# Performance work log

Measured on AMD Instinct MI355X. Metric: run time of the kernel, lower is better.

Reference implementation:

```python
import jax, jax.numpy as jnp
import numpy as np

N, E, F, H, G, C = 50000, 800000, 768, 256, 512, 2  # H = nhid*2 (nhid=128), G graphs, C classes
NHID = 128


def setup_inputs() -> dict:
    key = jax.random.key(0)
    ks = jax.random.split(key, 18)
    s = 0.05
    x = jax.random.normal(ks[0], (N, F), jnp.float32)
    edge_index = jax.random.randint(ks[1], (2, E), 0, N, dtype=jnp.int32)
    # sorted batch vector; every graph non-empty so the 'first node per graph' gather is valid
    batch = ((jnp.arange(N) * G) // N).astype(jnp.int32)
    return {
        "x": x,
        "edge_index": edge_index,
        "batch": batch,
        # GATConv 1 (in=F, out=H, heads=1)
        "W1": jax.random.normal(ks[2], (F, H), jnp.float32) * s,
        "as1": jax.random.normal(ks[3], (H,), jnp.float32) * s,
        "ad1": jax.random.normal(ks[4], (H,), jnp.float32) * s,
        "b1": jnp.zeros((H,), jnp.float32),
        # GATConv 2 (in=H, out=H)
        "W2": jax.random.normal(ks[5], (H, H), jnp.float32) * s,
        "as2": jax.random.normal(ks[6], (H,), jnp.float32) * s,
        "ad2": jax.random.normal(ks[7], (H,), jnp.float32) * s,
        "b2": jnp.zeros((H,), jnp.float32),
        # fc0: num_features -> nhid (news branch)
        "W0": jax.random.normal(ks[8], (F, NHID), jnp.float32) * s,
        "b0": jnp.zeros((NHID,), jnp.float32),
        # fc1: 2*nhid -> nhid (used twice, as in the source)
        "Wf1": jax.random.normal(ks[9], (H, NHID), jnp.float32) * s,
        "bf1": jnp.zeros((NHID,), jnp.float32),
        # fc2: nhid -> num_classes
        "Wf2": jax.random.normal(ks[10], (NHID, C), jnp.float32) * s,
        "bf2": jnp.zeros((C,), jnp.float32),
    }


def _gat(x, src, dst, W, a_s, a_d, b):
    # PyG GATConv, heads=1, concat=True, negative_slope=0.2, self-loops pre-appended to src/dst.
    h = x @ W                                   # [N, H]
    e = jax.nn.leaky_relu((h @ a_s)[src] + (h @ a_d)[dst], 0.2)  # [E+N]
    m = jax.ops.segment_max(e, dst, num_segments=N)
    ex = jnp.exp(e - m[dst])                    # stable segment softmax numerator
    denom = jax.ops.segment_sum(ex, dst, num_segments=N)
    agg = jax.ops.segment_sum(ex[:, None] * h[src], dst, num_segments=N)  # [N, H]
    return agg / denom[:, None] + b


def reference(x, edge_index, batch, W1, as1, ad1, b1, W2, as2, ad2, b2, W0, b0, Wf1, bf1, Wf2, bf2):
    loop = jnp.arange(N, dtype=edge_index.dtype)
    src = jnp.concatenate([edge_index[0], loop])  # add self-loops (PyG default)
    dst = jnp.concatenate([edge_index[1], loop])
    h = jax.nn.selu(_gat(x, src, dst, W1, as1, ad1, b1))
    h = jax.nn.selu(_gat(h, src, dst, W2, as2, ad2, b2))
    # global mean pool over graphs
    cnt = jax.ops.segment_sum(jnp.ones((N,), h.dtype), batch, num_segments=G)
    pooled = jax.nn.selu(jax.ops.segment_sum(h, batch, num_segments=G) / cnt[:, None])
    z = jax.nn.selu(pooled @ Wf1 + bf1)
    # dropout(p=0.5) in eval mode -> identity
    # concat branch: first node of each graph (news root)
    first_idx = jax.ops.segment_min(jnp.arange(N), batch, num_segments=G)
    news = jax.nn.relu(x[first_idx] @ W0 + b0)
    z = jnp.concatenate([z, news], axis=1)       # [G, 2*nhid]
    z = jax.nn.relu(z @ Wf1 + bf1)
    return jax.nn.log_softmax(z @ Wf2 + bf2, axis=-1)
```

## Files before the change

kernel.cpp:

```cpp
#include <hip/hip_runtime.h>
#include <hip/hip_bf16.h>
#include <cstdint>
#include <cstddef>

#define NN 50000
#define EE 800000
#define FF 768
#define HH 256
#define GG 512
#define CC 2
#define NHIDD 128
#define ETOT (EE + NN)
#define NCHUNK 49

typedef __attribute__((ext_vector_type(8))) short bf16x8;
typedef __attribute__((ext_vector_type(4))) float f32x4;
typedef __attribute__((ext_vector_type(8))) unsigned short us8;

__device__ __forceinline__ float b2f(unsigned short u){
  union { float f; uint32_t i; } v; v.i = ((uint32_t)u) << 16; return v.f;
}
__device__ __forceinline__ unsigned short f2b(float f){
  uint32_t u = __float_as_uint(f);
  uint32_t r = (u + 0x7fffu + ((u >> 16) & 1u)) >> 16;
  return (unsigned short)r;
}
__device__ __forceinline__ float selu_f(float x){
  const float lam = 1.0507009873554805f, alp = 1.6732632423543772f;
  return x > 0.f ? lam * x : lam * alp * (__expf(x) - 1.f);
}

__device__ __forceinline__ void gload_lds16(const unsigned short* g, unsigned short* l){
  __builtin_amdgcn_global_load_lds((const __attribute__((address_space(1))) void*)g,
                                   (__attribute__((address_space(3))) void*)l, 16, 0, 0);
}

__global__ __launch_bounds__(256) void xbf_kernel(const float* __restrict__ x, unsigned short* __restrict__ xb){
  size_t i = ((size_t)blockIdx.x * 256 + threadIdx.x) * 8;
  float4 f0 = *(const float4*)&x[i];
  float4 f1 = *(const float4*)&x[i + 4];
  us8 v;
  v[0] = f2b(f0.x); v[1] = f2b(f0.y); v[2] = f2b(f0.z); v[3] = f2b(f0.w);
  v[4] = f2b(f1.x); v[5] = f2b(f1.y); v[6] = f2b(f1.z); v[7] = f2b(f1.w);
  *(us8*)&xb[i] = v;
}

__global__ __launch_bounds__(256) void swizzleW(const float* __restrict__ W,
                                                unsigned short* __restrict__ Wsw, int K){
  int i = blockIdx.x * 256 + threadIdx.x;
  if (i < K * HH){
    int k = i / HH, n = i % HH;
    Wsw[(size_t)(k >> 5) * 8192 + n * 32 + (k & 31)] = f2b(W[i]);
  }
}

__global__ __launch_bounds__(256) void zero_deg(int* deg){
  int i = blockIdx.x * 256 + threadIdx.x;
  if (i < NN) deg[i] = 0;
}

__global__ __launch_bounds__(256) void deg_kernel(const int* __restrict__ dstA, int* __restrict__ deg){
  int i = blockIdx.x * 256 + threadIdx.x;
  if (i < ETOT){
    int d = (i < EE) ? dstA[i] : (i - EE);
    atomicAdd(&deg[d], 1);
  }
}

__global__ __launch_bounds__(256) void scanA(const int* __restrict__ deg, int* __restrict__ bsum){
  __shared__ int red[256];
  int c = blockIdx.x, tid = threadIdx.x;
  int base = c * 1024 + tid * 4;
  int s = 0;
#pragma unroll
  for (int j = 0; j < 4; j++){ int idx = base + j; if (idx < NN) s += deg[idx]; }
  red[tid] = s; __syncthreads();
  for (int off = 128; off > 0; off >>= 1){
    if (tid < off) red[tid] += red[tid + off];
    __syncthreads();
  }
  if (tid == 0) bsum[c] = red[0];
}

__global__ void scanB(int* bsum){
  if (threadIdx.x == 0){
    int run = 0;
    for (int i = 0; i < NCHUNK; i++){ int v = bsum[i]; bsum[i] = run; run += v; }
  }
}

__global__ __launch_bounds__(256) void scanC(const int* __restrict__ deg, const int* __restrict__ bsum,
                                             int* __restrict__ row_ptr, int* __restrict__ fill_ptr){
  __shared__ int ts[256];
  int c = blockIdx.x, tid = threadIdx.x;
  int base = c * 1024 + tid * 4;
  int v[4]; int s = 0;
#pragma unroll
  for (int j = 0; j < 4; j++){ int idx = base + j; v[j] = (idx < NN) ? deg[idx] : 0; s += v[j]; }
  ts[tid] = s; __syncthreads();
  for (int off = 1; off < 256; off <<= 1){
    int add = (tid >= off) ? ts[tid - off] : 0;
    __syncthreads();
    ts[tid] += add;
    __syncthreads();
  }
  int run = ts[tid] - s + bsum[c];
#pragma unroll
  for (int j = 0; j < 4; j++){
    int idx = base + j;
    if (idx < NN){ row_ptr[idx] = run; fill_ptr[idx] = run; }
    run += v[j];
  }
  if (c == 0 && tid == 0) row_ptr[NN] = ETOT;
}

__global__ __launch_bounds__(256) void fill_kernel(const int* __restrict__ srcA, const int* __restrict__ dstA,
                                                   int* __restrict__ fill_ptr, int* __restrict__ csr_src){
  int i = blockIdx.x * 256 + threadIdx.x;
  if (i < ETOT){
    int s = (i < EE) ? srcA[i] : (i - EE);
    int d = (i < EE) ? dstA[i] : (i - EE);
    int pos = atomicAdd(&fill_ptr[d], 1);
    csr_src[pos] = s;
  }
}

template<int K, int MINW>
__global__ __launch_bounds__(256, MINW) void gemm_mfma(const unsigned short* __restrict__ A,
                                                 const unsigned short* __restrict__ Wsw,
                                                 const float* __restrict__ a_s, const float* __restrict__ a_d,
                                                 unsigned short* __restrict__ out,
                                                 float* __restrict__ als, float* __restrict__ ald, int M){
  constexpr int CHROW = K / 8;
  __shared__ unsigned short Al[32 * K];
  const int tid = threadIdx.x;
  const int m0 = blockIdx.x * 32;
  const int lane = tid & 63, w = tid >> 6;
  const int koff = (lane >> 4) * 8;
  const int arow = lane & 15;
  const int nrow = w * 64 + (lane & 15);

  f32x4 acc[2][4];
#pragma unroll
  for (int rt = 0; rt < 2; rt++)
#pragma unroll
    for (int ct = 0; ct < 4; ct++) acc[rt][ct] = (f32x4){0.f, 0.f, 0.f, 0.f};

  constexpr int ROUNDS = (32 * CHROW) / 256;
#pragma unroll
  for (int j = 0; j < ROUNDS; j++){
    int L16 = j * 256 + tid;
    int row = L16 / CHROW;
    int ch  = L16 - row * CHROW;
    int sch = ch ^ (row & 7);
    int gr  = m0 + row; if (gr >= M) gr = M - 1;
    gload_lds16(A + (size_t)gr * K + sch * 8,
                &Al[(size_t)(j * 256 + w * 64) * 8]);
  }

  const unsigned short* bbase = Wsw + ((size_t)nrow * 32 + koff);
  bf16x8 bcur[2][4];
#pragma unroll
  for (int k2 = 0; k2 < 2; k2++)
#pragma unroll
    for (int ct = 0; ct < 4; ct++)
      bcur[k2][ct] = *(const bf16x8*)(bbase + (size_t)k2 * 8192 + ct * 512);

  __syncthreads();

  constexpr int NIT = K / 64;
  for (int ks = 0; ks < NIT; ks++){
    bf16x8 bnext[2][4];
    if (ks + 1 < NIT){
#pragma unroll
      for (int k2 = 0; k2 < 2; k2++)
#pragma unroll
        for (int ct = 0; ct < 4; ct++)
          bnext[k2][ct] = *(const bf16x8*)(bbase + (size_t)((ks + 1) * 2 + k2) * 8192 + ct * 512);
    }
    bf16x8 af[2][2];
#pragma unroll
    for (int k2 = 0; k2 < 2; k2++)
#pragma unroll
      for (int rt = 0; rt < 2; rt++){
        int R = rt * 16 + arow;
        int chb = (ks * 8 + k2 * 4 + (lane >> 4)) ^ (R & 7);
        af[k2][rt] = *(const bf16x8*)&Al[(size_t)R * K + chb * 8];
      }
#pragma unroll
    for (int k2 = 0; k2 < 2; k2++)
#pragma unroll
      for (int rt = 0; rt < 2; rt++)
#pragma unroll
        for (int ct = 0; ct < 4; ct++)
          acc[rt][ct] = __builtin_amdgcn_mfma_f32_16x16x32_bf16(af[k2][rt], bcur[k2][ct], acc[rt][ct], 0, 0, 0);
    if (ks + 1 < NIT){
#pragma unroll
      for (int k2 = 0; k2 < 2; k2++)
#pragma unroll
        for (int ct = 0; ct < 4; ct++) bcur[k2][ct] = bnext[k2][ct];
    }
  }

#pragma unroll
  for (int rt = 0; rt < 2; rt++){
    int mbase = m0 + rt * 16 + (lane >> 4) * 4;
#pragma unroll
    for (int r = 0; r < 4; r++){
      int m = mbase + r;
      if (m < M){
        size_t ro = (size_t)m * HH + w * 64 + (lane & 15);
        out[ro + 0]  = f2b(acc[rt][0][r]);
        out[ro + 16] = f2b(acc[rt][1][r]);
        out[ro + 32] = f2b(acc[rt][2][r]);
        out[ro + 48] = f2b(acc[rt][3][r]);
      }
    }
  }

  float as_c[4], ad_c[4];
#pragma unroll
  for (int ct = 0; ct < 4; ct++){
    int col = w * 64 + ct * 16 + (lane & 15);
    as_c[ct] = a_s[col]; ad_c[ct] = a_d[col];
  }
  float ps[2][4], pd[2][4];
#pragma unroll
  for (int rt = 0; rt < 2; rt++)
#pragma unroll
    for (int r = 0; r < 4; r++){
      float s = 0.f, d = 0.f;
#pragma unroll
      for (int ct = 0; ct < 4; ct++){ float v = acc[rt][ct][r]; s += v * as_c[ct]; d += v * ad_c[ct]; }
      ps[rt][r] = s; pd[rt][r] = d;
    }
#pragma unroll
  for (int off = 1; off < 16; off <<= 1){
#pragma unroll
    for (int rt = 0; rt < 2; rt++)
#pragma unroll
      for (int r = 0; r < 4; r++){
        ps[rt][r] += __shfl_xor(ps[rt][r], off);
        pd[rt][r] += __shfl_xor(pd[rt][r], off);
      }
  }
  __syncthreads();
  float* red = (float*)Al;
  if ((lane & 15) == 0){
    int q = lane >> 4;
#pragma unroll
    for (int rt = 0; rt < 2; rt++)
#pragma unroll
      for (int r = 0; r < 4; r++){
        int row = rt * 16 + q * 4 + r;
        red[w * 32 + row]       = ps[rt][r];
        red[128 + w * 32 + row] = pd[rt][r];
      }
  }
  __syncthreads();
  if (tid < 32){
    float s = red[tid] + red[32 + tid] + red[64 + tid] + red[96 + tid];
    float d = red[128 + tid] + red[160 + tid] + red[192 + tid] + red[224 + tid];
    int m = m0 + tid;
    if (m < M){ als[m] = s; ald[m] = d; }
  }
}

__global__ __launch_bounds__(256) void agg_wave(const unsigned short* __restrict__ h,
    const float* __restrict__ als, const float* __restrict__ ald,
    const int* __restrict__ row_ptr, const int* __restrict__ csr_src,
    const float* __restrict__ bias, unsigned short* __restrict__ outp){
  int node = blockIdx.x * 4 + (threadIdx.x >> 6);
  int lane = threadIdx.x & 63;
  if (node >= NN) return;
  int base = row_ptr[node];
  int deg  = row_ptr[node + 1] - base;
  float aldd = ald[node];
  float den = 0.f;
  float a0 = 0.f, a1 = 0.f, a2 = 0.f, a3 = 0.f;
  const size_t fo = (size_t)lane * 4;
  for (int p0 = 0; p0 < deg; p0 += 64){
    int cnt = min(64, deg - p0);
    float ev = 0.f; int s = 0;
    if (lane < cnt){
      s = csr_src[base + p0 + lane];
      float v = als[s] + aldd;
      v = v > 0.f ? v : 0.2f * v;
      ev = __expf(v);
    }
    den += ev;
    int j = 0;
    for (; j + 2 <= cnt; j += 2){
      float e0 = __shfl(ev, j), e1 = __shfl(ev, j + 1);
      int s0 = __shfl(s, j), s1 = __shfl(s, j + 1);
      ushort4 g0 = *(const ushort4*)&h[(size_t)s0 * HH + fo];
      ushort4 g1 = *(const ushort4*)&h[(size_t)s1 * HH + fo];
      a0 += e0 * b2f(g0.x) + e1 * b2f(g1.x);
      a1 += e0 * b2f(g0.y) + e1 * b2f(g1.y);
      a2 += e0 * b2f(g0.z) + e1 * b2f(g1.z);
      a3 += e0 * b2f(g0.w) + e1 * b2f(g1.w);
    }
    for (; j < cnt; j++){
      float e0 = __shfl(ev, j); int s0 = __shfl(s, j);
      ushort4 g0 = *(const ushort4*)&h[(size_t)s0 * HH + fo];
      a0 += e0 * b2f(g0.x); a1 += e0 * b2f(g0.y); a2 += e0 * b2f(g0.z); a3 += e0 * b2f(g0.w);
    }
  }
  for (int off = 32; off > 0; off >>= 1) den += __shfl_xor(den, off);
  float inv = 1.f / den;
  float4 b4 = *(const float4*)&bias[fo];
  ushort4 o;
  o.x = f2b(selu_f(a0 * inv + b4.x));
  o.y = f2b(selu_f(a1 * inv + b4.y));
  o.z = f2b(selu_f(a2 * inv + b4.z));
  o.w = f2b(selu_f(a3 * inv + b4.w));
  *(ushort4*)&outp[(size_t)node * HH + fo] = o;
}

__global__ __launch_bounds__(256) void first_kernel(const int* __restrict__ batch, int* __restrict__ first_idx){
  int n = blockIdx.x * 256 + threadIdx.x;
  if (n < NN){
    int b = batch[n];
    if (n == 0 || batch[n - 1] != b) first_idx[b] = n;
  }
  if (blockIdx.x == 0 && threadIdx.x == 0) first_idx[GG] = NN;
}

__global__ __launch_bounds__(256) void pool_kernel(const unsigned short* __restrict__ x3,
    const int* __restrict__ first_idx, float* __restrict__ pooled){
  int g = blockIdx.x, f = threadIdx.x;
  int s = first_idx[g], e = first_idx[g + 1];
  float acc = 0.f;
  for (int n = s; n < e; n++) acc += b2f(x3[(size_t)n * HH + f]);
  pooled[g * HH + f] = selu_f(acc / (float)(e - s));
}

__global__ __launch_bounds__(128) void z1_kernel(const float* __restrict__ pooled,
    const float* __restrict__ Wf1, const float* __restrict__ bf1,
    float* __restrict__ z1){
  __shared__ float pr[HH];
  int g = blockIdx.x, t = threadIdx.x;
  pr[t] = pooled[g * HH + t];
  pr[t + 128] = pooled[g * HH + t + 128];
  __syncthreads();
  float acc = 0.f;
  for (int k = 0; k < HH; k++) acc += pr[k] * Wf1[k * NHIDD + t];
  z1[g * NHIDD + t] = selu_f(acc + bf1[t]);
}

__global__ __launch_bounds__(128) void news_kernel(const float* __restrict__ x,
    const int* __restrict__ first_idx, const float* __restrict__ W0,
    const float* __restrict__ b0, float* __restrict__ znews){
  __shared__ float xr[FF];
  int g = blockIdx.x, t = threadIdx.x;
  int root = first_idx[g];
  for (int k = t; k < FF; k += 128) xr[k] = x[(size_t)root * FF + k];
  __syncthreads();
  float acc = 0.f;
  for (int k = 0; k < FF; k++) acc += xr[k] * W0[k * NHIDD + t];
  acc += b0[t];
  znews[g * NHIDD + t] = acc > 0.f ? acc : 0.f;
}

__global__ __launch_bounds__(128) void final_kernel(const float* __restrict__ z1,
    const float* __restrict__ znews, const float* __restrict__ Wf1,
    const float* __restrict__ bf1, const float* __restrict__ Wf2,
    const float* __restrict__ bf2, float* __restrict__ out){
  __shared__ float zc[HH];
  __shared__ float l0s[2], l1s[2];
  int g = blockIdx.x, t = threadIdx.x;
  zc[t] = z1[g * NHIDD + t];
  zc[NHIDD + t] = znews[g * NHIDD + t];
  __syncthreads();
  float acc = 0.f;
  for (int k = 0; k < HH; k++) acc += zc[k] * Wf1[k * NHIDD + t];
  float z2 = acc + bf1[t]; z2 = z2 > 0.f ? z2 : 0.f;
  float p0 = z2 * Wf2[t * CC + 0];
  float p1 = z2 * Wf2[t * CC + 1];
  for (int off = 32; off > 0; off >>= 1){ p0 += __shfl_xor(p0, off); p1 += __shfl_xor(p1, off); }
  int lane = t & 63, wid = t >> 6;
  if (lane == 0){ l0s[wid] = p0; l1s[wid] = p1; }
  __syncthreads();
  if (t == 0){
    float l0 = l0s[0] + l0s[1] + bf2[0];
    float l1 = l1s[0] + l1s[1] + bf2[1];
    float mx = fmaxf(l0, l1);
    float lse = mx + logf(__expf(l0 - mx) + __expf(l1 - mx));
    out[g * CC + 0] = l0 - lse;
    out[g * CC + 1] = l1 - lse;
  }
}

extern "C" void kernel_launch(void* const* d_in, const int* in_sizes, int n_in,
                              void* d_out, int out_size, void* d_ws, size_t ws_size,
                              hipStream_t stream){
  const float* x          = (const float*)d_in[0];
  const int* edge_index   = (const int*)d_in[1];
  const int* batch        = (const int*)d_in[2];
  const float* W1  = (const float*)d_in[3];
  const float* as1 = (const float*)d_in[4];
  const float* ad1 = (const float*)d_in[5];
  const float* b1  = (const float*)d_in[6];
  const float* W2  = (const float*)d_in[7];
  const float* as2 = (const float*)d_in[8];
  const float* ad2 = (const float*)d_in[9];
  const float* b2  = (const float*)d_in[10];
  const float* W0  = (const float*)d_in[11];
  const float* b0  = (const float*)d_in[12];
  const float* Wf1 = (const float*)d_in[13];
  const float* bf1 = (const float*)d_in[14];
  const float* Wf2 = (const float*)d_in[15];
  const float* bf2 = (const float*)d_in[16];
  float* out = (float*)d_out;

  char* w = (char*)d_ws;
  size_t off = 0;
  auto alloc = [&](size_t bytes){ size_t o = off; off += (bytes + 255) & ~(size_t)255; return o; };
  unsigned short* h    = (unsigned short*)(w + alloc((size_t)NN * HH * 2));
  unsigned short* x2   = (unsigned short*)(w + alloc((size_t)NN * HH * 2));
  unsigned short* xb   = (unsigned short*)(w + alloc((size_t)NN * FF * 2));
  unsigned short* Wsw1 = (unsigned short*)(w + alloc((size_t)FF * HH * 2));
  unsigned short* Wsw2 = (unsigned short*)(w + alloc((size_t)HH * HH * 2));
  float* als     = (float*)(w + alloc((size_t)NN * 4));
  float* ald     = (float*)(w + alloc((size_t)NN * 4));
  int*   deg     = (int*)(w + alloc((size_t)NN * 4));
  int*   row_ptr = (int*)(w + alloc((size_t)(NN + 1) * 4));
  int*   fillp   = (int*)(w + alloc((size_t)NN * 4));
  int*   csr_src = (int*)(w + alloc((size_t)ETOT * 4));
  int*   bsum    = (int*)(w + alloc(64 * 4));
  int*   firsti  = (int*)(w + alloc((size_t)(GG + 1) * 4));
  float* pooled  = (float*)(w + alloc((size_t)GG * HH * 4));
  float* z1      = (float*)(w + alloc((size_t)GG * NHIDD * 4));
  float* znews   = (float*)(w + alloc((size_t)GG * NHIDD * 4));

  const int* srcA = edge_index;
  const int* dstA = edge_index + EE;

  swizzleW<<<(FF * HH + 255) / 256, 256, 0, stream>>>(W1, Wsw1, FF);
  swizzleW<<<(HH * HH + 255) / 256, 256, 0, stream>>>(W2, Wsw2, HH);
  xbf_kernel<<<(NN * FF) / (256 * 8), 256, 0, stream>>>(x, xb);

  zero_deg<<<(NN + 255) / 256, 256, 0, stream>>>(deg);
  deg_kernel<<<(ETOT + 255) / 256, 256, 0, stream>>>(dstA, deg);
  scanA<<<NCHUNK, 256, 0, stream>>>(deg, bsum);
  scanB<<<1, 64, 0, stream>>>(bsum);
  scanC<<<NCHUNK, 256, 0, stream>>>(deg, bsum, row_ptr, fillp);
  fill_kernel<<<(ETOT + 255) / 256, 256, 0, stream>>>(srcA, dstA, fillp, csr_src);

  const int gemm_grid = (NN + 31) / 32;
  gemm_mfma<FF, 3><<<gemm_grid, 256, 0, stream>>>(xb, Wsw1, as1, ad1, h, als, ald, NN);
  agg_wave<<<(NN + 3) / 4, 256, 0, stream>>>(h, als, ald, row_ptr, csr_src, b1, x2);
  gemm_mfma<HH, 3><<<gemm_grid, 256, 0, stream>>>(x2, Wsw2, as2, ad2, h, als, ald, NN);
  agg_wave<<<(NN + 3) / 4, 256, 0, stream>>>(h, als, ald, row_ptr, csr_src, b2, x2);
  first_kernel<<<(NN + 255) / 256, 256, 0, stream>>>(batch, firsti);
  pool_kernel<<<GG, 256, 0, stream>>>(x2, firsti, pooled);
  z1_kernel<<<GG, 128, 0, stream>>>(pooled, Wf1, bf1, z1);
  news_kernel<<<GG, 128, 0, stream>>>(x, firsti, W0, b0, znews);
  final_kernel<<<GG, 128, 0, stream>>>(z1, znews, Wf1, bf1, Wf2, bf2, out);
}
```

Measured before the change: 629.1 us.

## Fuse scan phases, widen aggregation gathers, merge head kernels into one

Removes the single-thread scanB kernel by having each scanC block reduce the preceding chunk sums itself. Restructures agg_wave so each half-wave handles a different edge and gathers 8 bf16 features per lane with 16-byte loads, combining the halves with a cross-half shuffle at the end. Replaces first/pool/z1/news/final kernels with one head kernel that binary-searches graph bounds, pools, and runs the MLP head. Intent is fewer launches and wider memory transactions, at the cost of extra per-block scan work and more registers in aggregation.

```diff
diff --git a/kernel.cpp b/kernel.cpp
--- a/kernel.cpp
+++ b/kernel.cpp
@@ -82,17 +82,19 @@
   if (tid == 0) bsum[c] = red[0];
 }
 
-__global__ void scanB(int* bsum){
-  if (threadIdx.x == 0){
-    int run = 0;
-    for (int i = 0; i < NCHUNK; i++){ int v = bsum[i]; bsum[i] = run; run += v; }
-  }
-}
-
 __global__ __launch_bounds__(256) void scanC(const int* __restrict__ deg, const int* __restrict__ bsum,
                                              int* __restrict__ row_ptr, int* __restrict__ fill_ptr){
   __shared__ int ts[256];
+  __shared__ int cbase;
   int c = blockIdx.x, tid = threadIdx.x;
+  int pb = (tid < c) ? bsum[tid] : 0;
+  ts[tid] = pb; __syncthreads();
+  for (int off = 128; off > 0; off >>= 1){
+    if (tid < off) ts[tid] += ts[tid + off];
+    __syncthreads();
+  }
+  if (tid == 0) cbase = ts[0];
+  __syncthreads();
   int base = c * 1024 + tid * 4;
   int v[4]; int s = 0;
 #pragma unroll
@@ -104,7 +106,7 @@
     ts[tid] += add;
     __syncthreads();
   }
-  int run = ts[tid] - s + bsum[c];
+  int run = ts[tid] - s + cbase;
 #pragma unroll
   for (int j = 0; j < 4; j++){
     int idx = base + j;
@@ -277,8 +279,9 @@
   int deg  = row_ptr[node + 1] - base;
   float aldd = ald[node];
   float den = 0.f;
-  float a0 = 0.f, a1 = 0.f, a2 = 0.f, a3 = 0.f;
-  const size_t fo = (size_t)lane * 4;
+  float a[8] = {0.f, 0.f, 0.f, 0.f, 0.f, 0.f, 0.f, 0.f};
+  const int f8 = (lane & 31) * 8;
+  const int half = lane >> 5;
   for (int p0 = 0; p0 < deg; p0 += 64){
     int cnt = min(64, deg - p0);
     float ev = 0.f; int s = 0;
@@ -290,96 +293,92 @@
     }
     den += ev;
     int j = 0;
-    for (; j + 2 <= cnt; j += 2){
-      float e0 = __shfl(ev, j), e1 = __shfl(ev, j + 1);
-      int s0 = __shfl(s, j), s1 = __shfl(s, j + 1);
-      ushort4 g0 = *(const ushort4*)&h[(size_t)s0 * HH + fo];
-      ushort4 g1 = *(const ushort4*)&h[(size_t)s1 * HH + fo];
-      a0 += e0 * b2f(g0.x) + e1 * b2f(g1.x);
-      a1 += e0 * b2f(g0.y) + e1 * b2f(g1.y);
-      a2 += e0 * b2f(g0.z) + e1 * b2f(g1.z);
-      a3 += e0 * b2f(g0.w) + e1 * b2f(g1.w);
-    }
-    for (; j < cnt; j++){
-      float e0 = __shfl(ev, j); int s0 = __shfl(s, j);
-      ushort4 g0 = *(const ushort4*)&h[(size_t)s0 * HH + fo];
-      a0 += e0 * b2f(g0.x); a1 += e0 * b2f(g0.y); a2 += e0 * b2f(g0.z); a3 += e0 * b2f(g0.w);
+    for (; j + 4 <= cnt; j += 4){
+      int j0 = j + half, j1 = j + 2 + half;
+      int s0 = __shfl(s, j0), s1 = __shfl(s, j1);
+      float e0 = __shfl(ev, j0), e1 = __shfl(ev, j1);
+      us8 g0 = *(const us8*)&h[(size_t)s0 * HH + f8];
+      us8 g1 = *(const us8*)&h[(size_t)s1 * HH + f8];
+#pragma unroll
+      for (int i = 0; i < 8; i++) a[i] += e0 * b2f(g0[i]) + e1 * b2f(g1[i]);
+    }
+    for (; j < cnt; j += 2){
+      int jj = j + half;
+      int sj = __shfl(s, jj & 63);
+      float ejr = __shfl(ev, jj & 63);
+      float ej = (jj < cnt) ? ejr : 0.f;
+      us8 gj = *(const us8*)&h[(size_t)sj * HH + f8];
+#pragma unroll
+      for (int i = 0; i < 8; i++) a[i] += ej * b2f(gj[i]);
     }
   }
   for (int off = 32; off > 0; off >>= 1) den += __shfl_xor(den, off);
-  float inv = 1.f / den;
-  float4 b4 = *(const float4*)&bias[fo];
-  ushort4 o;
-  o.x = f2b(selu_f(a0 * inv + b4.x));
-  o.y = f2b(selu_f(a1 * inv + b4.y));
-  o.z = f2b(selu_f(a2 * inv + b4.z));
-  o.w = f2b(selu_f(a3 * inv + b4.w));
-  *(ushort4*)&outp[(size_t)node * HH + fo] = o;
-}
-
-__global__ __launch_bounds__(256) void first_kernel(const int* __restrict__ batch, int* __restrict__ first_idx){
-  int n = blockIdx.x * 256 + threadIdx.x;
-  if (n < NN){
-    int b = batch[n];
-    if (n == 0 || batch[n - 1] != b) first_idx[b] = n;
-  }
-  if (blockIdx.x == 0 && threadIdx.x == 0) first_idx[GG] = NN;
-}
-
-__global__ __launch_bounds__(256) void pool_kernel(const unsigned short* __restrict__ x3,
-    const int* __restrict__ first_idx, float* __restrict__ pooled){
-  int g = blockIdx.x, f = threadIdx.x;
-  int s = first_idx[g], e = first_idx[g + 1];
-  float acc = 0.f;
-  for (int n = s; n < e; n++) acc += b2f(x3[(size_t)n * HH + f]);
-  pooled[g * HH + f] = selu_f(acc / (float)(e - s));
-}
-
-__global__ __launch_bounds__(128) void z1_kernel(const float* __restrict__ pooled,
+#pragma unroll
+  for (int i = 0; i < 8; i++) a[i] += __shfl_xor(a[i], 32);
+  if (lane < 32){
+    float inv = 1.f / den;
+    float4 b4a = *(const float4*)&bias[f8];
+    float4 b4b = *(const float4*)&bias[f8 + 4];
+    us8 o;
+    o[0] = f2b(selu_f(a[0] * inv + b4a.x));
+    o[1] = f2b(selu_f(a[1] * inv + b4a.y));
+    o[2] = f2b(selu_f(a[2] * inv + b4a.z));
+    o[3] = f2b(selu_f(a[3] * inv + b4a.w));
+    o[4] = f2b(selu_f(a[4] * inv + b4b.x));
+    o[5] = f2b(selu_f(a[5] * inv + b4b.y));
+    o[6] = f2b(selu_f(a[6] * inv + b4b.z));
+    o[7] = f2b(selu_f(a[7] * inv + b4b.w));
+    *(us8*)&outp[(size_t)node * HH + f8] = o;
+  }
+}
+
+__global__ __launch_bounds__(256) void head_kernel(const unsigned short* __restrict__ x3,
+    const int* __restrict__ batch, const float* __restrict__ x,
+    const float* __restrict__ W0, const float* __restrict__ b0,
     const float* __restrict__ Wf1, const float* __restrict__ bf1,
-    float* __restrict__ z1){
+    const float* __restrict__ Wf2, const float* __restrict__ bf2,
+    float* __restrict__ out){
   __shared__ float pr[HH];
-  int g = blockIdx.x, t = threadIdx.x;
-  pr[t] = pooled[g * HH + t];
-  pr[t + 128] = pooled[g * HH + t + 128];
-  __syncthreads();
-  float acc = 0.f;
-  for (int k = 0; k < HH; k++) acc += pr[k] * Wf1[k * NHIDD + t];
-  z1[g * NHIDD + t] = selu_f(acc + bf1[t]);
-}
-
-__global__ __launch_bounds__(128) void news_kernel(const float* __restrict__ x,
-    const int* __restrict__ first_idx, const float* __restrict__ W0,
-    const float* __restrict__ b0, float* __restrict__ znews){
   __shared__ float xr[FF];
-  int g = blockIdx.x, t = threadIdx.x;
-  int root = first_idx[g];
-  for (int k = t; k < FF; k += 128) xr[k] = x[(size_t)root * FF + k];
-  __syncthreads();
-  float acc = 0.f;
-  for (int k = 0; k < FF; k++) acc += xr[k] * W0[k * NHIDD + t];
-  acc += b0[t];
-  znews[g * NHIDD + t] = acc > 0.f ? acc : 0.f;
-}
-
-__global__ __launch_bounds__(128) void final_kernel(const float* __restrict__ z1,
-    const float* __restrict__ znews, const float* __restrict__ Wf1,
-    const float* __restrict__ bf1, const float* __restrict__ Wf2,
-    const float* __restrict__ bf2, float* __restrict__ out){
   __shared__ float zc[HH];
+  __shared__ int se[2];
   __shared__ float l0s[2], l1s[2];
   int g = blockIdx.x, t = threadIdx.x;
-  zc[t] = z1[g * NHIDD + t];
-  zc[NHIDD + t] = znews[g * NHIDD + t];
-  __syncthreads();
-  float acc = 0.f;
-  for (int k = 0; k < HH; k++) acc += zc[k] * Wf1[k * NHIDD + t];
-  float z2 = acc + bf1[t]; z2 = z2 > 0.f ? z2 : 0.f;
-  float p0 = z2 * Wf2[t * CC + 0];
-  float p1 = z2 * Wf2[t * CC + 1];
-  for (int off = 32; off > 0; off >>= 1){ p0 += __shfl_xor(p0, off); p1 += __shfl_xor(p1, off); }
-  int lane = t & 63, wid = t >> 6;
-  if (lane == 0){ l0s[wid] = p0; l1s[wid] = p1; }
+  if (t < 2){
+    int target = g + t, lo = 0, hi = NN;
+    while (lo < hi){ int mid = (lo + hi) >> 1; if (batch[mid] < target) lo = mid + 1; else hi = mid; }
+    se[t] = lo;
+  }
+  __syncthreads();
+  int s = se[0], e = se[1];
+  {
+    float acc = 0.f;
+    for (int n = s; n < e; n++) acc += b2f(x3[(size_t)n * HH + t]);
+    pr[t] = selu_f(acc / (float)(e - s));
+  }
+  for (int k = t; k < FF; k += 256) xr[k] = x[(size_t)s * FF + k];
+  __syncthreads();
+  if (t < NHIDD){
+    float acc = 0.f;
+    for (int k = 0; k < HH; k++) acc += pr[k] * Wf1[k * NHIDD + t];
+    zc[t] = selu_f(acc + bf1[t]);
+  } else {
+    int t2 = t - NHIDD;
+    float acc = 0.f;
+    for (int k = 0; k < FF; k++) acc += xr[k] * W0[k * NHIDD + t2];
+    acc += b0[t2];
+    zc[NHIDD + t2] = acc > 0.f ? acc : 0.f;
+  }
+  __syncthreads();
+  if (t < NHIDD){
+    float acc = 0.f;
+    for (int k = 0; k < HH; k++) acc += zc[k] * Wf1[k * NHIDD + t];
+    float z2 = acc + bf1[t]; z2 = z2 > 0.f ? z2 : 0.f;
+    float p0 = z2 * Wf2[t * CC + 0];
+    float p1 = z2 * Wf2[t * CC + 1];
+    for (int off = 32; off > 0; off >>= 1){ p0 += __shfl_xor(p0, off); p1 += __shfl_xor(p1, off); }
+    if ((t & 63) == 0){ l0s[t >> 6] = p0; l1s[t >> 6] = p1; }
+  }
   __syncthreads();
   if (t == 0){
     float l0 = l0s[0] + l0s[1] + bf2[0];
@@ -428,10 +427,6 @@
   int*   fillp   = (int*)(w + alloc((size_t)NN * 4));
   int*   csr_src = (int*)(w + alloc((size_t)ETOT * 4));
   int*   bsum    = (int*)(w + alloc(64 * 4));
-  int*   firsti  = (int*)(w + alloc((size_t)(GG + 1) * 4));
-  float* pooled  = (float*)(w + alloc((size_t)GG * HH * 4));
-  float* z1      = (float*)(w + alloc((size_t)GG * NHIDD * 4));
-  float* znews   = (float*)(w + alloc((size_t)GG * NHIDD * 4));
 
   const int* srcA = edge_index;
   const int* dstA = edge_index + EE;
@@ -443,7 +438,6 @@
   zero_deg<<<(NN + 255) / 256, 256, 0, stream>>>(deg);
   deg_kernel<<<(ETOT + 255) / 256, 256, 0, stream>>>(dstA, deg);
   scanA<<<NCHUNK, 256, 0, stream>>>(deg, bsum);
-  scanB<<<1, 64, 0, stream>>>(bsum);
   scanC<<<NCHUNK, 256, 0, stream>>>(deg, bsum, row_ptr, fillp);
   fill_kernel<<<(ETOT + 255) / 256, 256, 0, stream>>>(srcA, dstA, fillp, csr_src);
 
@@ -452,9 +446,5 @@
   agg_wave<<<(NN + 3) / 4, 256, 0, stream>>>(h, als, ald, row_ptr, csr_src, b1, x2);
   gemm_mfma<HH, 3><<<gemm_grid, 256, 0, stream>>>(x2, Wsw2, as2, ad2, h, als, ald, NN);
   agg_wave<<<(NN + 3) / 4, 256, 0, stream>>>(h, als, ald, row_ptr, csr_src, b2, x2);
-  first_kernel<<<(NN + 255) / 256, 256, 0, stream>>>(batch, firsti);
-  pool_kernel<<<GG, 256, 0, stream>>>(x2, firsti, pooled);
-  z1_kernel<<<GG, 128, 0, stream>>>(pooled, Wf1, bf1, z1);
-  news_kernel<<<GG, 128, 0, stream>>>(x, firsti, W0, b0, znews);
-  final_kernel<<<GG, 128, 0, stream>>>(z1, znews, Wf1, bf1, Wf2, bf2, out);
-}
+  head_kernel<<<GG, 256, 0, stream>>>(x2, batch, x, W0, b0, Wf1, bf1, Wf2, bf2, out);
+}
```

After: 618.0 us. No clear change (-1.8%).
